# Optimization experiments

Measured on AMD Instinct MI355X. Metric: run time of the kernel, lower is better.

The kernel has to match this reference:

```python
import jax, jax.numpy as jnp
import numpy as np

D_MODEL = 512

def setup_inputs() -> dict:
    key = jax.random.key(0)
    ks = jax.random.split(key, 8)
    B, SQ, SKV, D = 4, 2048, 4096, D_MODEL
    scale = 1.0 / np.sqrt(D)
    return {
        "x": jax.random.normal(ks[0], (B, SQ, D), dtype=jnp.float32),
        "encoder_out": jax.random.normal(ks[1], (B, SKV, D), dtype=jnp.float32),
        "wq": jax.random.normal(ks[2], (D, D), dtype=jnp.float32) * scale,
        "bq": jax.random.normal(ks[3], (D,), dtype=jnp.float32) * 0.01,
        "wk": jax.random.normal(ks[4], (D, D), dtype=jnp.float32) * scale,
        "bk": jax.random.normal(ks[5], (D,), dtype=jnp.float32) * 0.01,
        "wv": jax.random.normal(ks[6], (D, D), dtype=jnp.float32) * scale,
        "bv": jax.random.normal(ks[7], (D,), dtype=jnp.float32) * 0.01,
    }

def reference(x, encoder_out, wq, bq, wk, bk, wv, bv):
    # torch Linear: y = x @ W.T + b
    q = jnp.einsum('bsd,ed->bse', x, wq) + bq            # [B,Sq,D]
    k = jnp.einsum('btd,ed->bte', encoder_out, wk) + bk  # [B,Skv,D]
    v = jnp.einsum('btd,ed->bte', encoder_out, wv) + bv  # [B,Skv,D]
    d_k = q.shape[-1]
    scores = jnp.einsum('bse,bte->bst', q, k) / jnp.sqrt(jnp.asarray(d_k, q.dtype))
    weights = jax.nn.softmax(scores, axis=-1)            # [B,Sq,Skv]
    return jnp.einsum('bst,bte->bse', weights, v)        # [B,Sq,D]
```

## Files before the change

kernel.cpp:

```cpp
#include <hip/hip_runtime.h>
#include <hip/hip_bf16.h>


typedef __bf16 bf16;
typedef __attribute__((ext_vector_type(8))) __bf16 bf16x8;
typedef __attribute__((ext_vector_type(4))) float f32x4;

#define DM 512

__device__ __forceinline__ void gload_lds16(const bf16* g, bf16* l)
{
    __builtin_amdgcn_global_load_lds(
        (const __attribute__((address_space(1))) void*)g,
        (__attribute__((address_space(3))) void*)l, 16, 0, 0);
}

__global__ __launch_bounds__(256) void cvt_all_kernel(
    const float* __restrict__ x,   bf16* __restrict__ xb,
    const float* __restrict__ enc, bf16* __restrict__ encb,
    const float* __restrict__ wq,  bf16* __restrict__ wqb,
    const float* __restrict__ wk,  bf16* __restrict__ wkb,
    const float* __restrict__ wv,  bf16* __restrict__ wvb)
{
    int g = blockIdx.x * 256 + threadIdx.x;
    const float* src; bf16* dst;
    if (g < 524288)       { src = x;   dst = xb; }
    else if (g < 1572864) { g -= 524288;  src = enc; dst = encb; }
    else if (g < 1605632) { g -= 1572864; src = wq;  dst = wqb; }
    else if (g < 1638400) { g -= 1605632; src = wk;  dst = wkb; }
    else                  { g -= 1638400; src = wv;  dst = wvb; }
    const float4 f0 = *reinterpret_cast<const float4*>(src + (size_t)g * 8);
    const float4 f1 = *reinterpret_cast<const float4*>(src + (size_t)g * 8 + 4);
    bf16x8 v;
    v[0]=(bf16)f0.x; v[1]=(bf16)f0.y; v[2]=(bf16)f0.z; v[3]=(bf16)f0.w;
    v[4]=(bf16)f1.x; v[5]=(bf16)f1.y; v[6]=(bf16)f1.z; v[7]=(bf16)f1.w;
    *reinterpret_cast<bf16x8*>(dst + (size_t)g * 8) = v;
}

template<bool KV>
__global__ __launch_bounds__(256) void proj_kernel(const bf16* __restrict__ A,
    const bf16* __restrict__ W0, const float* __restrict__ b0, bf16* __restrict__ out0,
    const bf16* __restrict__ W1, const float* __restrict__ b1, bf16* __restrict__ out1)
{
    __shared__ __align__(16) bf16 As[2][64][40];
    __shared__ __align__(16) bf16 W0s[2][64][40];
    __shared__ __align__(16) bf16 W1s[2][64][40];

    const int tid  = threadIdx.x;
    const int w    = tid >> 6, lane = tid & 63, quad = lane >> 4, l15 = lane & 15;
    const int wr   = w >> 1, wc = w & 1;
    const int n0   = blockIdx.x * 64;
    const int m0   = blockIdx.y * 64;
    const int srow = tid >> 2;
    const int scol = (tid & 3) * 8;

    f32x4 acc0[2][2] = {}, acc1[2][2] = {};
    bf16x8 ra, rw0, rw1;

    auto prefetch = [&](int kk) {
        ra  = *reinterpret_cast<const bf16x8*>(A  + (size_t)(m0 + srow) * DM + kk + scol);
        rw0 = *reinterpret_cast<const bf16x8*>(W0 + (size_t)(n0 + srow) * DM + kk + scol);
        if constexpr (KV)
            rw1 = *reinterpret_cast<const bf16x8*>(W1 + (size_t)(n0 + srow) * DM + kk + scol);
    };
    auto store_lds = [&](int p) {
        *reinterpret_cast<bf16x8*>(&As[p][srow][scol])  = ra;
        *reinterpret_cast<bf16x8*>(&W0s[p][srow][scol]) = rw0;
        if constexpr (KV)
            *reinterpret_cast<bf16x8*>(&W1s[p][srow][scol]) = rw1;
    };

    prefetch(0);
    store_lds(0);
    __syncthreads();

    for (int step = 0; step < 16; step++) {
        const int p = step & 1;
        if (step < 15) prefetch((step + 1) * 32);

        bf16x8 af[2], bf0[2], bf1[2];
#pragma unroll
        for (int mt = 0; mt < 2; mt++)
            af[mt] = *reinterpret_cast<const bf16x8*>(&As[p][32*wr + 16*mt + l15][quad*8]);
#pragma unroll
        for (int nt = 0; nt < 2; nt++)
            bf0[nt] = *reinterpret_cast<const bf16x8*>(&W0s[p][32*wc + 16*nt + l15][quad*8]);
        if constexpr (KV) {
#pragma unroll
            for (int nt = 0; nt < 2; nt++)
                bf1[nt] = *reinterpret_cast<const bf16x8*>(&W1s[p][32*wc + 16*nt + l15][quad*8]);
        }
#pragma unroll
        for (int mt = 0; mt < 2; mt++)
#pragma unroll
            for (int nt = 0; nt < 2; nt++) {
                acc0[mt][nt] = __builtin_amdgcn_mfma_f32_16x16x32_bf16(af[mt], bf0[nt], acc0[mt][nt], 0, 0, 0);
                if constexpr (KV)
                    acc1[mt][nt] = __builtin_amdgcn_mfma_f32_16x16x32_bf16(af[mt], bf1[nt], acc1[mt][nt], 0, 0, 0);
            }

        if (step < 15) store_lds(p ^ 1);
        __syncthreads();
    }

#pragma unroll
    for (int mt = 0; mt < 2; mt++)
#pragma unroll
        for (int nt = 0; nt < 2; nt++) {
            const int coll = 32*wc + 16*nt + l15;
            const int rowl = 32*wr + 16*mt + quad*4;
            {
                const float bv = b0[n0 + coll];
                f32x4 c = acc0[mt][nt];
#pragma unroll
                for (int r = 0; r < 4; r++)
                    out0[(size_t)(m0 + rowl + r) * DM + n0 + coll] = (bf16)(c[r] + bv);
            }
            if constexpr (KV) {
                const float bv = b1[n0 + coll];
                f32x4 c = acc1[mt][nt];
                const int gr = m0 + rowl;
                const int bidx = gr >> 12, t = gr & 4095;
                const int e = n0 + coll;
                union { uint2 u; bf16 h[4]; } pk;
#pragma unroll
                for (int r = 0; r < 4; r++) pk.h[r] = (bf16)(c[r] + bv);
                *reinterpret_cast<uint2*>(out1 +
                    ((((size_t)(bidx*128 + (t >> 5)) * DM + e) << 5) + (t & 31))) = pk.u;
            }
        }
}

__global__ __launch_bounds__(512, 2) void attn_kernel(const bf16* __restrict__ Qb,
                                                      const bf16* __restrict__ Kb,
                                                      const bf16* __restrict__ Vtg,
                                                      float* __restrict__ Op,
                                                      float* __restrict__ lp)
{
    __shared__ __align__(16) bf16 Kt[2][64][512];
    __shared__ __align__(16) bf16 Ps[64][80];
    __shared__ float lred[64];

    const int tid  = threadIdx.x;
    const int w    = tid >> 6, lane = tid & 63, quad = lane >> 4, l15 = lane & 15;
    const int qb   = w >> 1;
    const int cb0  = (w & 1) * 2;

    const int id = blockIdx.x;
    const int combo = id & 7, qblk = id >> 3;
    const int b = combo & 3, z = combo >> 2;
    const int q0 = qblk * 64;
    const int NT = 32, tb = z * 2048;

    bf16x8 af[16];
    {
        const bf16* qsrc = Qb + (size_t)(b*2048 + q0 + 16*qb + l15) * DM + quad*8;
#pragma unroll
        for (int k4 = 0; k4 < 16; k4++) af[k4] = *reinterpret_cast<const bf16x8*>(qsrc + k4*32);
    }
    if (tid < 64) lred[tid] = 0.f;

    const bf16* kbase = Kb + (size_t)(b*4096 + tb) * DM;
#pragma unroll
    for (int i = 0; i < 8; i++) {
        const int row = w + 8*i;
        gload_lds16(kbase + (size_t)row * DM + ((lane ^ (row & 15)) * 8), &Kt[0][row][0]);
    }
    __syncthreads();

    f32x4 oacc[4][4] = {};
    float lsum[2][4] = {};
    const float kexp = 1.44269504088896f * 0.044194173824159216f;
    const int sxor = l15 << 4;

    for (int t = 0; t < NT; t++) {
        const int buf = t & 1;

        bf16x8 vf[4][2];
#pragma unroll
        for (int ks = 0; ks < 2; ks++) {
            const size_t tblk = (size_t)(b*128 + z*64 + t*2 + ks) * DM;
#pragma unroll
            for (int nt = 0; nt < 4; nt++)
                vf[nt][ks] = *reinterpret_cast<const bf16x8*>(
                    Vtg + ((tblk + 64*w + 16*nt + l15) << 5) + quad*8);
        }

        if (t + 1 < NT) {
            const bf16* ksrc = kbase + (size_t)(t + 1) * 64 * DM;
#pragma unroll
            for (int i = 0; i < 8; i++) {
                const int row = w + 8*i;
                gload_lds16(ksrc + (size_t)row * DM + ((lane ^ (row & 15)) * 8), &Kt[buf ^ 1][row][0]);
            }
        }

        f32x4 sacc[2] = {};
        const char* krowA = (const char*)&Kt[buf][16*cb0 + l15][0];
        const char* krowB = (const char*)&Kt[buf][16*cb0 + 16 + l15][0];
#pragma unroll
        for (int k4 = 0; k4 < 16; k4++) {
            const int off = (k4*64 + quad*16) ^ sxor;
            bf16x8 k0 = *reinterpret_cast<const bf16x8*>(krowA + off);
            bf16x8 k1 = *reinterpret_cast<const bf16x8*>(krowB + off);
            sacc[0] = __builtin_amdgcn_mfma_f32_16x16x32_bf16(af[k4], k0, sacc[0], 0, 0, 0);
            sacc[1] = __builtin_amdgcn_mfma_f32_16x16x32_bf16(af[k4], k1, sacc[1], 0, 0, 0);
        }

#pragma unroll
        for (int s = 0; s < 2; s++)
#pragma unroll
            for (int r = 0; r < 4; r++) {
                const float p = exp2f(sacc[s][r] * kexp);
                lsum[s][r] += p;
                Ps[16*qb + quad*4 + r][16*(cb0 + s) + l15] = (bf16)p;
            }

        asm volatile("s_waitcnt lgkmcnt(0)" ::: "memory");
        __builtin_amdgcn_s_barrier();
        __builtin_amdgcn_sched_barrier(0);

#pragma unroll
        for (int ks = 0; ks < 2; ks++) {
            bf16x8 ap[4];
#pragma unroll
            for (int mt = 0; mt < 4; mt++)
                ap[mt] = *reinterpret_cast<const bf16x8*>(&Ps[16*mt + l15][ks*32 + quad*8]);
#pragma unroll
            for (int nt = 0; nt < 4; nt++)
#pragma unroll
                for (int mt = 0; mt < 4; mt++)
                    oacc[mt][nt] = __builtin_amdgcn_mfma_f32_16x16x32_bf16(ap[mt], vf[nt][ks], oacc[mt][nt], 0, 0, 0);
        }
        __syncthreads();
    }

#pragma unroll
    for (int r = 0; r < 4; r++)
        atomicAdd(&lred[16*qb + quad*4 + r], lsum[0][r] + lsum[1][r]);
    __syncthreads();

    if (tid < 64) lp[(size_t)z * 8192 + b * 2048 + q0 + tid] = lred[tid];
#pragma unroll
    for (int mt = 0; mt < 4; mt++)
#pragma unroll
        for (int r = 0; r < 4; r++) {
            const int row = 16*mt + quad*4 + r;
            float* obase = Op + ((size_t)z * 8192 + b * 2048 + q0 + row) * DM;
#pragma unroll
            for (int nt = 0; nt < 4; nt++)
                obase[64*w + 16*nt + l15] = oacc[mt][nt][r];
        }
}

__global__ __launch_bounds__(256) void reduce_kernel(const float* __restrict__ Op,
                                                     const float* __restrict__ lp,
                                                     float* __restrict__ out)
{
    const int g = blockIdx.x * 256 + threadIdx.x;
    const size_t e = (size_t)g * 4;
    const int row = g >> 7;
    float4 o = *reinterpret_cast<const float4*>(Op + e);
    float4 a = *reinterpret_cast<const float4*>(Op + 4194304 + e);
    const float l = lp[row] + lp[8192 + row];
    const float linv = 1.0f / l;
    o.x = (o.x + a.x) * linv;
    o.y = (o.y + a.y) * linv;
    o.z = (o.z + a.z) * linv;
    o.w = (o.w + a.w) * linv;
    *reinterpret_cast<float4*>(out + e) = o;
}

extern "C" void kernel_launch(void* const* d_in, const int* in_sizes, int n_in,
                              void* d_out, int out_size, void* d_ws, size_t ws_size,
                              hipStream_t stream)
{
    const float* x   = (const float*)d_in[0];
    const float* enc = (const float*)d_in[1];
    const float* wq  = (const float*)d_in[2];
    const float* bq  = (const float*)d_in[3];
    const float* wk  = (const float*)d_in[4];
    const float* bk  = (const float*)d_in[5];
    const float* wv  = (const float*)d_in[6];
    const float* bv  = (const float*)d_in[7];
    float* out = (float*)d_out;

    char* ws = (char*)d_ws;
    bf16*  Qb   = (bf16*)ws;
    bf16*  Kb   = (bf16*)(ws + 8388608);
    bf16*  Vtg  = (bf16*)(ws + 25165824);
    bf16*  xb   = (bf16*)(ws + 41943040);
    bf16*  encb = (bf16*)(ws + 50331648);
    bf16*  wqb  = (bf16*)(ws + 67108864);
    bf16*  wkb  = (bf16*)(ws + 67633152);
    bf16*  wvb  = (bf16*)(ws + 68157440);
    float* Op   = (float*)(ws + 41943040);
    float* lp   = (float*)(ws + 41943040 + 2ull * 16777216);

    hipLaunchKernelGGL(cvt_all_kernel, dim3(6528), dim3(256), 0, stream,
                       x, xb, enc, encb, wq, wqb, wk, wkb, wv, wvb);

    hipLaunchKernelGGL((proj_kernel<false>), dim3(8, 128), dim3(256), 0, stream,
                       xb, wqb, bq, Qb, (const bf16*)nullptr, (const float*)nullptr, (bf16*)nullptr);
    hipLaunchKernelGGL((proj_kernel<true>),  dim3(8, 256), dim3(256), 0, stream,
                       encb, wkb, bk, Kb, wvb, bv, Vtg);

    hipLaunchKernelGGL(attn_kernel, dim3(256), dim3(512), 0, stream, Qb, Kb, Vtg, Op, lp);
    hipLaunchKernelGGL(reduce_kernel, dim3(4096), dim3(256), 0, stream, Op, lp, out);
}
```

Before: 242.0 us.

## Enlarge projection GEMM tiles to 128x128 with direct-to-LDS loads and XOR swizzle

The Q/K/V projection kernel moves from 64x64 tiles to 128x128 tiles with 4x4 MFMA subtiles per wave, which raises reuse of each LDS fragment and halves the grid in each dimension. Global-to-shared staging now uses global_load_lds DMA instead of a register round trip. The LDS rows lose their padding and use an XOR column swizzle to avoid bank conflicts. The larger accumulator set, 32 f32x4 in the KV variant, raises register pressure, and the smaller grid may underfill the device.

```diff
diff --git a/kernel.cpp b/kernel.cpp
--- a/kernel.cpp
+++ b/kernel.cpp
@@ -38,77 +38,76 @@
 }
 
 template<bool KV>
-__global__ __launch_bounds__(256) void proj_kernel(const bf16* __restrict__ A,
+__global__ __launch_bounds__(256, 2) void proj_kernel(const bf16* __restrict__ A,
     const bf16* __restrict__ W0, const float* __restrict__ b0, bf16* __restrict__ out0,
     const bf16* __restrict__ W1, const float* __restrict__ b1, bf16* __restrict__ out1)
 {
-    __shared__ __align__(16) bf16 As[2][64][40];
-    __shared__ __align__(16) bf16 W0s[2][64][40];
-    __shared__ __align__(16) bf16 W1s[2][64][40];
+    __shared__ __align__(16) bf16 As[2][128][32];
+    __shared__ __align__(16) bf16 W0s[2][128][32];
+    __shared__ __align__(16) bf16 W1s[2][128][32];
 
     const int tid  = threadIdx.x;
     const int w    = tid >> 6, lane = tid & 63, quad = lane >> 4, l15 = lane & 15;
     const int wr   = w >> 1, wc = w & 1;
-    const int n0   = blockIdx.x * 64;
-    const int m0   = blockIdx.y * 64;
-    const int srow = tid >> 2;
-    const int scol = (tid & 3) * 8;
-
-    f32x4 acc0[2][2] = {}, acc1[2][2] = {};
-    bf16x8 ra, rw0, rw1;
-
-    auto prefetch = [&](int kk) {
-        ra  = *reinterpret_cast<const bf16x8*>(A  + (size_t)(m0 + srow) * DM + kk + scol);
-        rw0 = *reinterpret_cast<const bf16x8*>(W0 + (size_t)(n0 + srow) * DM + kk + scol);
-        if constexpr (KV)
-            rw1 = *reinterpret_cast<const bf16x8*>(W1 + (size_t)(n0 + srow) * DM + kk + scol);
+    const int n0   = blockIdx.x * 128;
+    const int m0   = blockIdx.y * 128;
+
+    const int lrow = lane >> 2;
+    const int scol = ((lane & 3) ^ (lrow & 3)) * 8;
+    const bf16* aSrc  = A  + (size_t)(m0 + lrow) * DM + scol;
+    const bf16* wSrc0 = W0 + (size_t)(n0 + lrow) * DM + scol;
+    const bf16* wSrc1 = KV ? (W1 + (size_t)(n0 + lrow) * DM + scol) : nullptr;
+
+    auto stage = [&](int p, int kk) {
+#pragma unroll
+        for (int j = 0; j < 2; j++) {
+            const int seg = 2 * w + j;
+            gload_lds16(aSrc  + (size_t)(16 * seg) * DM + kk, &As[p][16 * seg][0]);
+            gload_lds16(wSrc0 + (size_t)(16 * seg) * DM + kk, &W0s[p][16 * seg][0]);
+            if constexpr (KV)
+                gload_lds16(wSrc1 + (size_t)(16 * seg) * DM + kk, &W1s[p][16 * seg][0]);
+        }
     };
-    auto store_lds = [&](int p) {
-        *reinterpret_cast<bf16x8*>(&As[p][srow][scol])  = ra;
-        *reinterpret_cast<bf16x8*>(&W0s[p][srow][scol]) = rw0;
-        if constexpr (KV)
-            *reinterpret_cast<bf16x8*>(&W1s[p][srow][scol]) = rw1;
-    };
-
-    prefetch(0);
-    store_lds(0);
+
+    f32x4 acc0[4][4] = {}, acc1[4][4] = {};
+    const int sx = (l15 & 3);
+
+    stage(0, 0);
     __syncthreads();
 
     for (int step = 0; step < 16; step++) {
         const int p = step & 1;
-        if (step < 15) prefetch((step + 1) * 32);
-
-        bf16x8 af[2], bf0[2], bf1[2];
-#pragma unroll
-        for (int mt = 0; mt < 2; mt++)
-            af[mt] = *reinterpret_cast<const bf16x8*>(&As[p][32*wr + 16*mt + l15][quad*8]);
-#pragma unroll
-        for (int nt = 0; nt < 2; nt++)
-            bf0[nt] = *reinterpret_cast<const bf16x8*>(&W0s[p][32*wc + 16*nt + l15][quad*8]);
-        if constexpr (KV) {
-#pragma unroll
-            for (int nt = 0; nt < 2; nt++)
-                bf1[nt] = *reinterpret_cast<const bf16x8*>(&W1s[p][32*wc + 16*nt + l15][quad*8]);
-        }
-#pragma unroll
-        for (int mt = 0; mt < 2; mt++)
-#pragma unroll
-            for (int nt = 0; nt < 2; nt++) {
-                acc0[mt][nt] = __builtin_amdgcn_mfma_f32_16x16x32_bf16(af[mt], bf0[nt], acc0[mt][nt], 0, 0, 0);
-                if constexpr (KV)
-                    acc1[mt][nt] = __builtin_amdgcn_mfma_f32_16x16x32_bf16(af[mt], bf1[nt], acc1[mt][nt], 0, 0, 0);
-            }
-
-        if (step < 15) store_lds(p ^ 1);
+        if (step < 15) stage(p ^ 1, (step + 1) * 32);
+
+        bf16x8 af[4];
+#pragma unroll
+        for (int mt = 0; mt < 4; mt++)
+            af[mt] = *reinterpret_cast<const bf16x8*>(
+                &As[p][64*wr + 16*mt + l15][(quad ^ sx) * 8]);
+#pragma unroll
+        for (int nt = 0; nt < 4; nt++) {
+            bf16x8 w0f = *reinterpret_cast<const bf16x8*>(
+                &W0s[p][64*wc + 16*nt + l15][(quad ^ sx) * 8]);
+#pragma unroll
+            for (int mt = 0; mt < 4; mt++)
+                acc0[mt][nt] = __builtin_amdgcn_mfma_f32_16x16x32_bf16(af[mt], w0f, acc0[mt][nt], 0, 0, 0);
+            if constexpr (KV) {
+                bf16x8 w1f = *reinterpret_cast<const bf16x8*>(
+                    &W1s[p][64*wc + 16*nt + l15][(quad ^ sx) * 8]);
+#pragma unroll
+                for (int mt = 0; mt < 4; mt++)
+                    acc1[mt][nt] = __builtin_amdgcn_mfma_f32_16x16x32_bf16(af[mt], w1f, acc1[mt][nt], 0, 0, 0);
+            }
+        }
         __syncthreads();
     }
 
 #pragma unroll
-    for (int mt = 0; mt < 2; mt++)
-#pragma unroll
-        for (int nt = 0; nt < 2; nt++) {
-            const int coll = 32*wc + 16*nt + l15;
-            const int rowl = 32*wr + 16*mt + quad*4;
+    for (int mt = 0; mt < 4; mt++)
+#pragma unroll
+        for (int nt = 0; nt < 4; nt++) {
+            const int coll = 64*wc + 16*nt + l15;
+            const int rowl = 64*wr + 16*mt + quad*4;
             {
                 const float bv = b0[n0 + coll];
                 f32x4 c = acc0[mt][nt];
@@ -300,9 +299,9 @@
     hipLaunchKernelGGL(cvt_all_kernel, dim3(6528), dim3(256), 0, stream,
                        x, xb, enc, encb, wq, wqb, wk, wkb, wv, wvb);
 
-    hipLaunchKernelGGL((proj_kernel<false>), dim3(8, 128), dim3(256), 0, stream,
+    hipLaunchKernelGGL((proj_kernel<false>), dim3(4, 64), dim3(256), 0, stream,
                        xb, wqb, bq, Qb, (const bf16*)nullptr, (const float*)nullptr, (bf16*)nullptr);
-    hipLaunchKernelGGL((proj_kernel<true>),  dim3(8, 256), dim3(256), 0, stream,
+    hipLaunchKernelGGL((proj_kernel<true>),  dim3(4, 128), dim3(256), 0, stream,
                        encb, wkb, bk, Kb, wvb, bv, Vtg);
 
     hipLaunchKernelGGL(attn_kernel, dim3(256), dim3(512), 0, stream, Qb, Kb, Vtg, Op, lp);
```

New measurement: 232.0 us. 4.1% less time.
